# Kernel tuning notes

Measured on AMD Instinct MI355X. Metric: run time of the kernel, lower is better.

The kernel has to match this reference:

```python
import jax, jax.numpy as jnp
import numpy as np

B, S, D_IN, D_OUT, H = 4, 2048, 1024, 1024, 16
HD = D_OUT // H


def setup_inputs() -> dict:
    key = jax.random.key(0)
    ks = jax.random.split(key, 6)
    sc_in = 1.0 / np.sqrt(D_IN)
    sc_out = 1.0 / np.sqrt(D_OUT)
    return {
        "x": jax.random.normal(ks[0], (B, S, D_IN), dtype=jnp.float32),
        "Wq": jax.random.normal(ks[1], (D_IN, D_OUT), dtype=jnp.float32) * sc_in,
        "Wk": jax.random.normal(ks[2], (D_IN, D_OUT), dtype=jnp.float32) * sc_in,
        "Wv": jax.random.normal(ks[3], (D_IN, D_OUT), dtype=jnp.float32) * sc_in,
        "Wo": jax.random.normal(ks[4], (D_OUT, D_OUT), dtype=jnp.float32) * sc_out,
        "bo": jax.random.normal(ks[5], (D_OUT,), dtype=jnp.float32) * 0.01,
    }


def reference(x, Wq, Wk, Wv, Wo, bo):
    b, s, _ = x.shape
    # projections -> [b, h, s, hd]
    def split_heads(t):
        return t.reshape(b, s, H, HD).transpose(0, 2, 1, 3)
    q = split_heads(x @ Wq)
    k = split_heads(x @ Wk)
    v = split_heads(x @ Wv)
    # full score matrix [b, h, s, s], causal mask, scaled softmax
    scores = jnp.einsum("bhqd,bhkd->bhqk", q, k)
    causal = jnp.tril(jnp.ones((s, s), dtype=bool))
    scores = jnp.where(causal, scores, -jnp.inf)
    attn = jax.nn.softmax(scores / np.sqrt(HD), axis=-1)
    # dropout p=0.0 -> identity
    ctx = jnp.einsum("bhqk,bhkd->bhqd", attn, v)
    ctx = ctx.transpose(0, 2, 1, 3).reshape(b, s, D_OUT)
    return ctx @ Wo + bo
```

## Files before the change

### kernel.cpp

```cpp
#include <hip/hip_runtime.h>


typedef float  f32x4  __attribute__((ext_vector_type(4)));
typedef __bf16 bf16x8 __attribute__((ext_vector_type(8)));
typedef __bf16 bf16x4 __attribute__((ext_vector_type(4)));

#define AS(n) __attribute__((address_space(n)))

__device__ __forceinline__ void gload16(const void* g, void* l) {
    __builtin_amdgcn_global_load_lds((const AS(1) void*)g, (AS(3) void*)l, 16, 0, 0);
}

__device__ __forceinline__ f32x4 mfma16(bf16x8 a, bf16x8 b, f32x4 c) {
    return __builtin_amdgcn_mfma_f32_16x16x32_bf16(a, b, c, 0, 0, 0);
}

__global__ void convert_x_kernel(const float4* __restrict__ x, __bf16* __restrict__ xb) {
    int t = blockIdx.x * 256 + threadIdx.x;
    float4 v = x[t];
    bf16x4 o = { (__bf16)v.x, (__bf16)v.y, (__bf16)v.z, (__bf16)v.w };
    ((bf16x4*)xb)[t] = o;
}

__global__ void transpose_w_kernel(const float* __restrict__ Wq, const float* __restrict__ Wk,
                                   const float* __restrict__ Wv, const float* __restrict__ Wo,
                                   __bf16* __restrict__ wqkvt, __bf16* __restrict__ wot) {
    const float* src; __bf16* dst;
    int z = blockIdx.z;
    if (z == 0)      { src = Wq; dst = wqkvt; }
    else if (z == 1) { src = Wk; dst = wqkvt + 1048576; }
    else if (z == 2) { src = Wv; dst = wqkvt + 2097152; }
    else             { src = Wo; dst = wot; }
    __shared__ float tile[32][33];
    int tx = threadIdx.x, ty = threadIdx.y;
    int x = blockIdx.x * 32 + tx;
    int y0 = blockIdx.y * 32;
#pragma unroll
    for (int i = ty; i < 32; i += 8) tile[i][tx] = src[(size_t)(y0 + i) * 1024 + x];
    __syncthreads();
    int xo = blockIdx.y * 32 + tx;
    int yo0 = blockIdx.x * 32;
#pragma unroll
    for (int i = ty; i < 32; i += 8) dst[(size_t)(yo0 + i) * 1024 + xo] = (__bf16)tile[tx][i];
}

__global__ __launch_bounds__(256, 2) void gemm_qkv_kernel(
        const __bf16* __restrict__ A, const __bf16* __restrict__ Bt,
        __bf16* __restrict__ Qp, __bf16* __restrict__ Kp, __bf16* __restrict__ Vp) {
    __shared__ __bf16 lA[128 * 32];
    __shared__ __bf16 lB[128 * 32];
    int tid = threadIdx.x;
    int m0 = blockIdx.x * 128, n0 = blockIdx.y * 128;
    int w = tid >> 6, lane = tid & 63, quad = lane >> 4, l15 = lane & 15;
    int wm = (w & 1) * 64, wn = (w >> 1) * 64;
    f32x4 acc[4][4] = {};
    int rowS = tid >> 2, kc = tid & 3;
    const __bf16* Abase = A + (size_t)m0 * 1024;
    const __bf16* Bbase = Bt + (size_t)n0 * 1024;
    for (int kt = 0; kt < 32; kt++) {
        int k0 = kt * 32;
        gload16(Abase + (size_t)rowS * 1024 + k0 + kc * 8,        &lA[tid * 8]);
        gload16(Abase + (size_t)(rowS + 64) * 1024 + k0 + kc * 8, &lA[(tid + 256) * 8]);
        gload16(Bbase + (size_t)rowS * 1024 + k0 + kc * 8,        &lB[tid * 8]);
        gload16(Bbase + (size_t)(rowS + 64) * 1024 + k0 + kc * 8, &lB[(tid + 256) * 8]);
        __syncthreads();
        bf16x8 a[4], b[4];
#pragma unroll
        for (int i = 0; i < 4; i++) a[i] = *(const bf16x8*)&lA[(wm + i * 16 + l15) * 32 + quad * 8];
#pragma unroll
        for (int j = 0; j < 4; j++) b[j] = *(const bf16x8*)&lB[(wn + j * 16 + l15) * 32 + quad * 8];
#pragma unroll
        for (int i = 0; i < 4; i++)
#pragma unroll
            for (int j = 0; j < 4; j++)
                acc[i][j] = mfma16(a[i], b[j], acc[i][j]);
        __syncthreads();
    }
    int mat = n0 >> 10;
    int ncol0 = n0 & 1023;
    __bf16* dst = (mat == 0) ? Qp : ((mat == 1) ? Kp : Vp);
    float sc = (mat == 0) ? 0.1803368801111204f : 1.0f;
#pragma unroll
    for (int i = 0; i < 4; i++) {
#pragma unroll
        for (int j = 0; j < 4; j++) {
            int n = ncol0 + wn + j * 16 + l15;
            int h = n >> 6, d = n & 63;
#pragma unroll
            for (int r = 0; r < 4; r++) {
                int m = m0 + wm + i * 16 + quad * 4 + r;
                int bb = m >> 11, s = m & 2047;
                dst[((((size_t)bb * 16 + h) * 2048 + s) << 6) + d] = (__bf16)(acc[i][j][r] * sc);
            }
        }
    }
}

__global__ __launch_bounds__(256, 2) void attn_kernel(
        const __bf16* __restrict__ Q, const __bf16* __restrict__ K,
        const __bf16* __restrict__ V, __bf16* __restrict__ ctx) {
    int xb = blockIdx.x;
    int bh = blockIdx.y;
    int b = bh >> 4, h = bh & 15;
    const __bf16* Qb = Q + (size_t)bh * (2048 * 64);
    const __bf16* Kb = K + (size_t)bh * (2048 * 64);
    const __bf16* Vb = V + (size_t)bh * (2048 * 64);
    __shared__ __bf16 sK[64 * 72];
    __shared__ __bf16 sV[64 * 72];
    __shared__ __bf16 sP[128 * 72];
    int tid = threadIdx.x, w = tid >> 6, lane = tid & 63, quad = lane >> 4, l15 = lane & 15;
    int srow = tid >> 2, scol = tid & 3;
    int vkey = srow ^ (scol << 4);
    const bf16x8 vone = { (__bf16)1.0f, (__bf16)1.0f, (__bf16)1.0f, (__bf16)1.0f,
                          (__bf16)1.0f, (__bf16)1.0f, (__bf16)1.0f, (__bf16)1.0f };

    for (int half = 0; half < 2; half++) {
        int qt = half ? (15 - xb) : xb;
        int q0 = qt * 128;
        int nkt = 2 * qt + 2;
        bf16x8 aQ[2][2];
#pragma unroll
        for (int h2 = 0; h2 < 2; h2++)
#pragma unroll
            for (int c = 0; c < 2; c++)
                aQ[h2][c] = *(const bf16x8*)(Qb + (size_t)(q0 + w * 32 + h2 * 16 + l15) * 64 + c * 32 + quad * 8);
        f32x4 o[2][4] = {};
        f32x4 lac[2] = {};
        const __bf16* ksrc0 = Kb + srow * 64 + scol * 16;
        const __bf16* vsrc0 = Vb + srow * 64 + scol * 16;
        bf16x8 kA = *(const bf16x8*)ksrc0;
        bf16x8 kB = *(const bf16x8*)(ksrc0 + 8);
        bf16x8 vA = *(const bf16x8*)vsrc0;
        bf16x8 vB = *(const bf16x8*)(vsrc0 + 8);
        for (int kt = 0; kt < nkt; kt++) {
            *(bf16x8*)&sK[srow * 72 + scol * 16]     = kA;
            *(bf16x8*)&sK[srow * 72 + scol * 16 + 8] = kB;
#pragma unroll
            for (int e = 0; e < 8; e++) sV[(scol * 16 + e) * 72 + vkey]     = vA[e];
#pragma unroll
            for (int e = 0; e < 8; e++) sV[(scol * 16 + 8 + e) * 72 + vkey] = vB[e];
            __syncthreads();
            if (kt + 1 < nkt) {
                const __bf16* kp = Kb + ((kt + 1) * 64 + srow) * 64 + scol * 16;
                const __bf16* vp = Vb + ((kt + 1) * 64 + srow) * 64 + scol * 16;
                kA = *(const bf16x8*)kp;  kB = *(const bf16x8*)(kp + 8);
                vA = *(const bf16x8*)vp;  vB = *(const bf16x8*)(vp + 8);
            }
            int mb = kt * 64 - q0;
            bool diag = (kt >= 2 * qt);
            if (!(diag && (mb - w * 32 >= 32))) {
                f32x4 s[2][4] = {};
#pragma unroll
                for (int c = 0; c < 2; c++)
#pragma unroll
                    for (int j = 0; j < 4; j++) {
                        bf16x8 kf = *(const bf16x8*)&sK[(j * 16 + l15) * 72 + c * 32 + quad * 8];
                        s[0][j] = mfma16(aQ[0][c], kf, s[0][j]);
                        s[1][j] = mfma16(aQ[1][c], kf, s[1][j]);
                    }
                if (diag && (mb + 63 > w * 32)) {
#pragma unroll
                    for (int h2 = 0; h2 < 2; h2++)
#pragma unroll
                        for (int j = 0; j < 4; j++) {
                            int key = j * 16 + l15 + mb;
#pragma unroll
                            for (int r = 0; r < 4; r++)
                                if (key > w * 32 + h2 * 16 + quad * 4 + r) s[h2][j][r] = -1e30f;
                        }
                }
#pragma unroll
                for (int h2 = 0; h2 < 2; h2++)
#pragma unroll
                    for (int j = 0; j < 4; j++)
#pragma unroll
                        for (int r = 0; r < 4; r++)
                            s[h2][j][r] = exp2f(s[h2][j][r]);
#pragma unroll
                for (int h2 = 0; h2 < 2; h2++)
#pragma unroll
                    for (int j = 0; j < 4; j++) {
                        int kg = ((j ^ quad) << 4) + l15;
#pragma unroll
                        for (int r = 0; r < 4; r++)
                            sP[(w * 32 + h2 * 16 + quad * 4 + r) * 72 + kg] = (__bf16)s[h2][j][r];
                    }
                int pswz = (l15 >> 2) << 4;
#pragma unroll
                for (int h2 = 0; h2 < 2; h2++) {
                    int prow = (w * 32 + h2 * 16 + l15) * 72;
                    bf16x8 p0 = *(const bf16x8*)&sP[prow + ((quad * 8) ^ pswz)];
                    bf16x8 p1 = *(const bf16x8*)&sP[prow + ((quad * 8 + 32) ^ pswz)];
                    lac[h2] = mfma16(p0, vone, lac[h2]);
                    lac[h2] = mfma16(p1, vone, lac[h2]);
#pragma unroll
                    for (int dj = 0; dj < 4; dj++) {
                        int vrow = (dj * 16 + l15) * 72;
                        int vswz = dj << 4;
                        bf16x8 v0 = *(const bf16x8*)&sV[vrow + ((quad * 8) ^ vswz)];
                        bf16x8 v1 = *(const bf16x8*)&sV[vrow + ((quad * 8 + 32) ^ vswz)];
                        f32x4 t = mfma16(p0, v0, o[h2][dj]);
                        o[h2][dj] = mfma16(p1, v1, t);
                    }
                }
            }
            __syncthreads();
        }
#pragma unroll
        for (int h2 = 0; h2 < 2; h2++)
#pragma unroll
            for (int r = 0; r < 4; r++) {
                float inv = 1.0f / lac[h2][r];
                int q = q0 + w * 32 + h2 * 16 + quad * 4 + r;
                size_t base = (((size_t)b * 2048 + q) << 10) + h * 64;
#pragma unroll
                for (int dj = 0; dj < 4; dj++)
                    ctx[base + dj * 16 + l15] = (__bf16)(o[h2][dj][r] * inv);
            }
    }
}

__global__ __launch_bounds__(256, 2) void gemm_out_kernel(
        const __bf16* __restrict__ A, const __bf16* __restrict__ Bt,
        const float* __restrict__ bo, float* __restrict__ out) {
    __shared__ __bf16 lA[128 * 32];
    __shared__ __bf16 lB[128 * 32];
    int tid = threadIdx.x;
    int m0 = blockIdx.x * 128, n0 = blockIdx.y * 128;
    int w = tid >> 6, lane = tid & 63, quad = lane >> 4, l15 = lane & 15;
    int wm = (w & 1) * 64, wn = (w >> 1) * 64;
    f32x4 acc[4][4] = {};
    int rowS = tid >> 2, kc = tid & 3;
    const __bf16* Abase = A + (size_t)m0 * 1024;
    const __bf16* Bbase = Bt + (size_t)n0 * 1024;
    for (int kt = 0; kt < 32; kt++) {
        int k0 = kt * 32;
        gload16(Abase + (size_t)rowS * 1024 + k0 + kc * 8,        &lA[tid * 8]);
        gload16(Abase + (size_t)(rowS + 64) * 1024 + k0 + kc * 8, &lA[(tid + 256) * 8]);
        gload16(Bbase + (size_t)rowS * 1024 + k0 + kc * 8,        &lB[tid * 8]);
        gload16(Bbase + (size_t)(rowS + 64) * 1024 + k0 + kc * 8, &lB[(tid + 256) * 8]);
        __syncthreads();
        bf16x8 a[4], b[4];
#pragma unroll
        for (int i = 0; i < 4; i++) a[i] = *(const bf16x8*)&lA[(wm + i * 16 + l15) * 32 + quad * 8];
#pragma unroll
        for (int j = 0; j < 4; j++) b[j] = *(const bf16x8*)&lB[(wn + j * 16 + l15) * 32 + quad * 8];
#pragma unroll
        for (int i = 0; i < 4; i++)
#pragma unroll
            for (int j = 0; j < 4; j++)
                acc[i][j] = mfma16(a[i], b[j], acc[i][j]);
        __syncthreads();
    }
#pragma unroll
    for (int j = 0; j < 4; j++) {
        int n = n0 + wn + j * 16 + l15;
        float bias = bo[n];
#pragma unroll
        for (int i = 0; i < 4; i++)
#pragma unroll
            for (int r = 0; r < 4; r++) {
                int m = m0 + wm + i * 16 + quad * 4 + r;
                out[(size_t)m * 1024 + n] = acc[i][j][r] + bias;
            }
    }
}

extern "C" void kernel_launch(void* const* d_in, const int* in_sizes, int n_in,
                              void* d_out, int out_size, void* d_ws, size_t ws_size,
                              hipStream_t stream) {
    const float* x  = (const float*)d_in[0];
    const float* Wq = (const float*)d_in[1];
    const float* Wk = (const float*)d_in[2];
    const float* Wv = (const float*)d_in[3];
    const float* Wo = (const float*)d_in[4];
    const float* bo = (const float*)d_in[5];
    float* out = (float*)d_out;

    __bf16* ws    = (__bf16*)d_ws;
    __bf16* xb    = ws;
    __bf16* wqkvt = xb + 8388608;
    __bf16* wot   = wqkvt + 3145728;
    __bf16* Qp    = wot + 1048576;
    __bf16* Kp    = Qp + 8388608;
    __bf16* Vp    = Kp + 8388608;
    __bf16* ctx   = Vp + 8388608;

    convert_x_kernel<<<8192, 256, 0, stream>>>((const float4*)x, xb);
    transpose_w_kernel<<<dim3(32, 32, 4), dim3(32, 8), 0, stream>>>(Wq, Wk, Wv, Wo, wqkvt, wot);
    gemm_qkv_kernel<<<dim3(64, 24), 256, 0, stream>>>(xb, wqkvt, Qp, Kp, Vp);
    attn_kernel<<<dim3(8, 64), 256, 0, stream>>>(Qp, Kp, Vp, ctx);
    gemm_out_kernel<<<dim3(64, 8), 256, 0, stream>>>(ctx, wot, bo, out);
}
```

Measured before the change: 272.7 us.

## Pre-transpose V in a separate kernel and double-buffer K/V tiles in attention

Adds a kernel that transposes V to a [bh, d, s] layout, written into the now-unused x buffer, so the attention kernel can store V tiles to LDS with vector writes. Before, each thread did sixteen scalar swizzled stores per tile. The attention loop now double-buffers the K and V shared tiles and writes the next tile after compute, which removes the trailing barrier in each iteration. The cost is an extra kernel launch, an extra pass over V in global memory, and twice the LDS for K/V, which may lower occupancy.

```diff
diff --git a/kernel.cpp b/kernel.cpp
--- a/kernel.cpp
+++ b/kernel.cpp
@@ -96,21 +96,42 @@
     }
 }
 
+__global__ void transpose_v_kernel(const __bf16* __restrict__ Vp, __bf16* __restrict__ Vt) {
+    int st = blockIdx.x;
+    int bh = blockIdx.y;
+    __shared__ __bf16 t[64 * 72];
+    int tid = threadIdx.x;
+    const __bf16* src = Vp + (((size_t)bh * 2048) + st * 64) * 64;
+    int s = tid >> 2, c = tid & 3;
+    *(bf16x8*)&t[s * 72 + c * 16]     = *(const bf16x8*)(src + s * 64 + c * 16);
+    *(bf16x8*)&t[s * 72 + c * 16 + 8] = *(const bf16x8*)(src + s * 64 + c * 16 + 8);
+    __syncthreads();
+    int d = tid >> 2, c2 = tid & 3;
+    bf16x8 o1, o2;
+#pragma unroll
+    for (int e = 0; e < 8; e++) o1[e] = t[(c2 * 16 + e) * 72 + d];
+#pragma unroll
+    for (int e = 0; e < 8; e++) o2[e] = t[(c2 * 16 + 8 + e) * 72 + d];
+    __bf16* dst = Vt + (((size_t)bh * 64) + d) * 2048 + st * 64 + c2 * 16;
+    *(bf16x8*)dst = o1;
+    *(bf16x8*)(dst + 8) = o2;
+}
+
 __global__ __launch_bounds__(256, 2) void attn_kernel(
         const __bf16* __restrict__ Q, const __bf16* __restrict__ K,
-        const __bf16* __restrict__ V, __bf16* __restrict__ ctx) {
+        const __bf16* __restrict__ Vt, __bf16* __restrict__ ctx) {
     int xb = blockIdx.x;
     int bh = blockIdx.y;
     int b = bh >> 4, h = bh & 15;
-    const __bf16* Qb = Q + (size_t)bh * (2048 * 64);
-    const __bf16* Kb = K + (size_t)bh * (2048 * 64);
-    const __bf16* Vb = V + (size_t)bh * (2048 * 64);
-    __shared__ __bf16 sK[64 * 72];
-    __shared__ __bf16 sV[64 * 72];
+    const __bf16* Qb = Q  + (size_t)bh * (2048 * 64);
+    const __bf16* Kb = K  + (size_t)bh * (2048 * 64);
+    const __bf16* Vb = Vt + (size_t)bh * (64 * 2048);
+    __shared__ __bf16 sK[2][64 * 72];
+    __shared__ __bf16 sV[2][64 * 72];
     __shared__ __bf16 sP[128 * 72];
     int tid = threadIdx.x, w = tid >> 6, lane = tid & 63, quad = lane >> 4, l15 = lane & 15;
     int srow = tid >> 2, scol = tid & 3;
-    int vkey = srow ^ (scol << 4);
+    int vd = tid >> 2, vc = tid & 3;
     const bf16x8 vone = { (__bf16)1.0f, (__bf16)1.0f, (__bf16)1.0f, (__bf16)1.0f,
                           (__bf16)1.0f, (__bf16)1.0f, (__bf16)1.0f, (__bf16)1.0f };
 
@@ -126,23 +147,26 @@
                 aQ[h2][c] = *(const bf16x8*)(Qb + (size_t)(q0 + w * 32 + h2 * 16 + l15) * 64 + c * 32 + quad * 8);
         f32x4 o[2][4] = {};
         f32x4 lac[2] = {};
-        const __bf16* ksrc0 = Kb + srow * 64 + scol * 16;
-        const __bf16* vsrc0 = Vb + srow * 64 + scol * 16;
-        bf16x8 kA = *(const bf16x8*)ksrc0;
-        bf16x8 kB = *(const bf16x8*)(ksrc0 + 8);
-        bf16x8 vA = *(const bf16x8*)vsrc0;
-        bf16x8 vB = *(const bf16x8*)(vsrc0 + 8);
+        if (half) __syncthreads();
+        {
+            const __bf16* kp = Kb + srow * 64 + scol * 16;
+            const __bf16* vp = Vb + (size_t)vd * 2048 + vc * 16;
+            bf16x8 kA = *(const bf16x8*)kp;
+            bf16x8 kB = *(const bf16x8*)(kp + 8);
+            bf16x8 vA = *(const bf16x8*)vp;
+            bf16x8 vB = *(const bf16x8*)(vp + 8);
+            *(bf16x8*)&sK[0][srow * 72 + scol * 16]     = kA;
+            *(bf16x8*)&sK[0][srow * 72 + scol * 16 + 8] = kB;
+            *(bf16x8*)&sV[0][vd * 72 + vc * 16]         = vA;
+            *(bf16x8*)&sV[0][vd * 72 + vc * 16 + 8]     = vB;
+        }
         for (int kt = 0; kt < nkt; kt++) {
-            *(bf16x8*)&sK[srow * 72 + scol * 16]     = kA;
-            *(bf16x8*)&sK[srow * 72 + scol * 16 + 8] = kB;
-#pragma unroll
-            for (int e = 0; e < 8; e++) sV[(scol * 16 + e) * 72 + vkey]     = vA[e];
-#pragma unroll
-            for (int e = 0; e < 8; e++) sV[(scol * 16 + 8 + e) * 72 + vkey] = vB[e];
+            int cur = kt & 1;
             __syncthreads();
+            bf16x8 kA, kB, vA, vB;
             if (kt + 1 < nkt) {
                 const __bf16* kp = Kb + ((kt + 1) * 64 + srow) * 64 + scol * 16;
-                const __bf16* vp = Vb + ((kt + 1) * 64 + srow) * 64 + scol * 16;
+                const __bf16* vp = Vb + (size_t)vd * 2048 + (kt + 1) * 64 + vc * 16;
                 kA = *(const bf16x8*)kp;  kB = *(const bf16x8*)(kp + 8);
                 vA = *(const bf16x8*)vp;  vB = *(const bf16x8*)(vp + 8);
             }
@@ -154,7 +178,7 @@
                 for (int c = 0; c < 2; c++)
 #pragma unroll
                     for (int j = 0; j < 4; j++) {
-                        bf16x8 kf = *(const bf16x8*)&sK[(j * 16 + l15) * 72 + c * 32 + quad * 8];
+                        bf16x8 kf = *(const bf16x8*)&sK[cur][(j * 16 + l15) * 72 + c * 32 + quad * 8];
                         s[0][j] = mfma16(aQ[0][c], kf, s[0][j]);
                         s[1][j] = mfma16(aQ[1][c], kf, s[1][j]);
                     }
@@ -196,15 +220,19 @@
 #pragma unroll
                     for (int dj = 0; dj < 4; dj++) {
                         int vrow = (dj * 16 + l15) * 72;
-                        int vswz = dj << 4;
-                        bf16x8 v0 = *(const bf16x8*)&sV[vrow + ((quad * 8) ^ vswz)];
-                        bf16x8 v1 = *(const bf16x8*)&sV[vrow + ((quad * 8 + 32) ^ vswz)];
+                        bf16x8 v0 = *(const bf16x8*)&sV[cur][vrow + quad * 8];
+                        bf16x8 v1 = *(const bf16x8*)&sV[cur][vrow + quad * 8 + 32];
                         f32x4 t = mfma16(p0, v0, o[h2][dj]);
                         o[h2][dj] = mfma16(p1, v1, t);
                     }
                 }
             }
-            __syncthreads();
+            if (kt + 1 < nkt) {
+                *(bf16x8*)&sK[1 - cur][srow * 72 + scol * 16]     = kA;
+                *(bf16x8*)&sK[1 - cur][srow * 72 + scol * 16 + 8] = kB;
+                *(bf16x8*)&sV[1 - cur][vd * 72 + vc * 16]         = vA;
+                *(bf16x8*)&sV[1 - cur][vd * 72 + vc * 16 + 8]     = vB;
+            }
         }
 #pragma unroll
         for (int h2 = 0; h2 < 2; h2++)
@@ -285,10 +313,12 @@
     __bf16* Kp    = Qp + 8388608;
     __bf16* Vp    = Kp + 8388608;
     __bf16* ctx   = Vp + 8388608;
+    __bf16* Vt    = xb;
 
     convert_x_kernel<<<8192, 256, 0, stream>>>((const float4*)x, xb);
     transpose_w_kernel<<<dim3(32, 32, 4), dim3(32, 8), 0, stream>>>(Wq, Wk, Wv, Wo, wqkvt, wot);
     gemm_qkv_kernel<<<dim3(64, 24), 256, 0, stream>>>(xb, wqkvt, Qp, Kp, Vp);
-    attn_kernel<<<dim3(8, 64), 256, 0, stream>>>(Qp, Kp, Vp, ctx);
+    transpose_v_kernel<<<dim3(32, 64), 256, 0, stream>>>(Vp, Vt);
+    attn_kernel<<<dim3(8, 64), 256, 0, stream>>>(Qp, Kp, Vt, ctx);
     gemm_out_kernel<<<dim3(64, 8), 256, 0, stream>>>(ctx, wot, bo, out);
 }
```

New measurement: 272.4 us. Within noise of the previous version (-0.1%).
